# Kernel tuning notes

Hardware: AMD Instinct MI355X
Metric: run time of the kernel (lower is better)

The kernel has to match this reference:

```python
import jax, jax.numpy as jnp
import numpy as np

B, T, C = 4, 2048, 1024
H = 16
D = C // H  # head_dim = 64
SCALE = D ** -0.5


def setup_inputs() -> dict:
    key = jax.random.key(0)
    k1, k2, k3 = jax.random.split(key, 3)
    x = jax.random.normal(k1, (B, T, C), dtype=jnp.float32)
    w_qkv = jax.random.normal(k2, (C, 3 * C), dtype=jnp.float32) * (C ** -0.5)
    w_proj = jax.random.normal(k3, (C, C), dtype=jnp.float32) * (C ** -0.5)
    return {"x": x, "w_qkv": w_qkv, "w_proj": w_proj}


def reference(x, w_qkv, w_proj):
    Bx, Tx, Cx = x.shape
    qkv = x @ w_qkv                        # [B, T, 3C]
    q, k, v = jnp.split(qkv, 3, axis=-1)   # each [B, T, C]
    # [B, T, H, D] -> [B, H, T, D]
    q = q.reshape(Bx, Tx, H, D).transpose(0, 2, 1, 3)
    k = k.reshape(Bx, Tx, H, D).transpose(0, 2, 1, 3)
    v = v.reshape(Bx, Tx, H, D).transpose(0, 2, 1, 3)
    att = jnp.einsum('bhqd,bhkd->bhqk', q, k) * SCALE  # [B, H, T, T]
    causal = jnp.tril(jnp.ones((Tx, Tx), dtype=bool))
    att = jnp.where(causal[None, None], att, -jnp.inf)
    att = jax.nn.softmax(att, axis=-1)
    # dropout p=0.0 (eval-mode reference): identity
    y = jnp.einsum('bhqk,bhkd->bhqd', att, v)          # [B, H, T, D]
    y = y.transpose(0, 2, 1, 3).reshape(Bx, Tx, Cx)    # [B, T, C]
    return y @ w_proj
```

## Files before the change

### kernel.cpp

```cpp
#include <hip/hip_runtime.h>
#include <hip/hip_bf16.h>

#define Bdim 4
#define Tdim 2048
#define Cdim 1024
#define Hdim 16
#define Ddim 64
#define SCALE_Q 0.125f

using f32x4  = __attribute__((ext_vector_type(4))) float;
using short8 = __attribute__((ext_vector_type(8))) short;

union U8 { uint4 v; unsigned short s[8]; };

__device__ __forceinline__ float bf2f(unsigned short u) {
  union { unsigned int i; float f; } x; x.i = ((unsigned int)u) << 16; return x.f;
}
__device__ __forceinline__ unsigned short f2bf(float f) {
  union { float f; unsigned int i; } x; x.f = f;
  unsigned int lsb = (x.i >> 16) & 1u;
  unsigned int r = x.i + 0x7fffu + lsb;
  return (unsigned short)(r >> 16);
}

__device__ __forceinline__ void glds16(const unsigned short* g, unsigned short* l) {
  __builtin_amdgcn_global_load_lds(
      (const __attribute__((address_space(1))) void*)g,
      (__attribute__((address_space(3))) void*)l,
      16, 0, 0);
}

__device__ __forceinline__ int detect_fmt(const unsigned int* xw) {
  int cnt = 0;
  for (int i = 0; i < 64; i++) {
    unsigned int e = (xw[i] >> 7) & 0xFFu;
    if (e >= 100u && e <= 140u) cnt++;
  }
  return (cnt >= 40) ? 1 : 0;
}

__global__ void detect_kernel(const unsigned int* __restrict__ x, int* __restrict__ flag) {
  if (threadIdx.x == 0) *flag = detect_fmt(x);
}

__global__ __launch_bounds__(256) void prep_kernel(
    const void* __restrict__ x, const void* __restrict__ wq, const void* __restrict__ wp,
    unsigned short* __restrict__ X16, unsigned short* __restrict__ WqT,
    unsigned short* __restrict__ WpT, int* __restrict__ flag)
{
  __shared__ __align__(16) unsigned short Ts[64][72];
  __shared__ int sfmt;
  if (threadIdx.x == 0) {
    const int f = detect_fmt((const unsigned int*)x);
    sfmt = f;
    if (blockIdx.x == 0) *flag = f;
  }
  __syncthreads();
  const int fmt = sfmt;
  const unsigned bid = blockIdx.x;
  const int tid = threadIdx.x;

  if (bid < 4096u) {
    const size_t i = (size_t)bid * 256 + tid;
    if (fmt == 1) {
      *(uint4*)(X16 + i * 8) = *(const uint4*)((const unsigned short*)x + i * 8);
    } else {
      const float* s = (const float*)x + i * 8;
      float4 a = *(const float4*)(s);
      float4 b = *(const float4*)(s + 4);
      U8 o;
      o.s[0]=f2bf(a.x); o.s[1]=f2bf(a.y); o.s[2]=f2bf(a.z); o.s[3]=f2bf(a.w);
      o.s[4]=f2bf(b.x); o.s[5]=f2bf(b.y); o.s[6]=f2bf(b.z); o.s[7]=f2bf(b.w);
      *(uint4*)(X16 + i * 8) = o.v;
    }
    return;
  }

  const void* W; unsigned short* WT; int N, K, n0, k0;
  if (bid < 4864u) {
    const int t = bid - 4096;
    W = wq; WT = WqT; N = 3072; K = 1024;
    n0 = (t % 48) * 64; k0 = (t / 48) * 64;
  } else {
    const int t = bid - 4864;
    W = wp; WT = WpT; N = 1024; K = 1024;
    n0 = (t & 15) * 64; k0 = (t >> 4) * 64;
  }
  const int r = tid >> 2, c0 = (tid & 3) * 16;

  if (fmt == 0) {
    const float* Wf = (const float*)W + (size_t)(k0 + r) * N + n0 + c0;
    #pragma unroll
    for (int j4 = 0; j4 < 4; j4++) {
      float4 v = *(const float4*)(Wf + j4 * 4);
      Ts[r][c0 + j4*4 + 0] = f2bf(v.x);
      Ts[r][c0 + j4*4 + 1] = f2bf(v.y);
      Ts[r][c0 + j4*4 + 2] = f2bf(v.z);
      Ts[r][c0 + j4*4 + 3] = f2bf(v.w);
    }
  } else {
    const unsigned short* Wh = (const unsigned short*)W + (size_t)(k0 + r) * N + n0 + c0;
    uint4 v0 = *(const uint4*)(Wh);
    uint4 v1 = *(const uint4*)(Wh + 8);
    *(uint4*)&Ts[r][c0] = v0;
    *(uint4*)&Ts[r][c0 + 8] = v1;
  }
  __syncthreads();

  U8 o0, o1;
  #pragma unroll
  for (int j = 0; j < 8; j++) { o0.s[j] = Ts[c0 + j][r]; o1.s[j] = Ts[c0 + 8 + j][r]; }
  unsigned short* dst = WT + (size_t)(n0 + r) * K + k0 + c0;
  *(uint4*)(dst)     = o0.v;
  *(uint4*)(dst + 8) = o1.v;
}

__global__ __launch_bounds__(256) void vtrans_kernel(
    const unsigned short* __restrict__ Vb, unsigned short* __restrict__ VbT)
{
  __shared__ __align__(16) unsigned short Ts[64][72];
  const int tid = threadIdx.x;
  const int head = blockIdx.x >> 5;
  const int tt   = blockIdx.x & 31;
  const int r = tid >> 2, c0 = (tid & 3) * 16;

  const unsigned short* src = Vb + (size_t)head * Tdim * Ddim + (size_t)(tt * 64 + r) * Ddim + c0;
  uint4 a = *(const uint4*)(src);
  uint4 b = *(const uint4*)(src + 8);
  *(uint4*)&Ts[r][c0]     = a;
  *(uint4*)&Ts[r][c0 + 8] = b;
  __syncthreads();

  U8 o0, o1;
  #pragma unroll
  for (int j = 0; j < 8; j++) { o0.s[j] = Ts[c0 + j][r]; o1.s[j] = Ts[c0 + 8 + j][r]; }
  unsigned short* dst = VbT + (size_t)head * Tdim * Ddim + (size_t)r * Tdim + tt * 64 + c0;
  *(uint4*)(dst)     = o0.v;
  *(uint4*)(dst + 8) = o1.v;
}

__global__ __launch_bounds__(256) void gemm128b_kernel(
    const unsigned short* __restrict__ A16,
    const unsigned short* __restrict__ BT16,
    void* __restrict__ Cout,
    unsigned short* __restrict__ Qb,
    unsigned short* __restrict__ Kb,
    unsigned short* __restrict__ Vb,
    const int* __restrict__ flag,
    int M, int N, int K, int mode)
{
  __shared__ __align__(16) unsigned short As[2][128 * 32];
  __shared__ __align__(16) unsigned short Bs[2][128 * 32];

  const int fmt = *flag;
  const int tid  = threadIdx.x;
  const int wave = tid >> 6;
  const int lane = tid & 63;
  const int col  = lane & 15;
  const int quad = lane >> 4;
  const int m0 = blockIdx.x * 128;
  const int n0 = blockIdx.y * 128;
  const int wm = (wave >> 1) * 64;
  const int wn = (wave & 1) * 64;

  const int lr = lane >> 2;
  const int lc = (lane & 3) * 8;

  f32x4 acc[4][4];
  #pragma unroll
  for (int i = 0; i < 4; i++)
    #pragma unroll
    for (int j = 0; j < 4; j++) acc[i][j] = (f32x4){0.f, 0.f, 0.f, 0.f};

  const unsigned short* Ap0 = A16  + (size_t)(m0 + wave * 32 + lr) * K + lc;
  const unsigned short* Ap1 = A16  + (size_t)(m0 + wave * 32 + 16 + lr) * K + lc;
  const unsigned short* Bp0 = BT16 + (size_t)(n0 + wave * 32 + lr) * K + lc;
  const unsigned short* Bp1 = BT16 + (size_t)(n0 + wave * 32 + 16 + lr) * K + lc;
  unsigned short* a0 = &As[0][wave * 32 * 32];
  unsigned short* a0b = &As[0][(wave * 32 + 16) * 32];
  unsigned short* a1 = &As[1][wave * 32 * 32];
  unsigned short* a1b = &As[1][(wave * 32 + 16) * 32];
  unsigned short* b0 = &Bs[0][wave * 32 * 32];
  unsigned short* b0b = &Bs[0][(wave * 32 + 16) * 32];
  unsigned short* b1 = &Bs[1][wave * 32 * 32];
  unsigned short* b1b = &Bs[1][(wave * 32 + 16) * 32];

  for (int k0 = 0; k0 < K; k0 += 64) {
    glds16(Ap0,      a0);  glds16(Ap0 + 32, a1);
    glds16(Ap1,      a0b); glds16(Ap1 + 32, a1b);
    glds16(Bp0,      b0);  glds16(Bp0 + 32, b1);
    glds16(Bp1,      b0b); glds16(Bp1 + 32, b1b);
    Ap0 += 64; Ap1 += 64; Bp0 += 64; Bp1 += 64;
    __syncthreads();

    #pragma unroll
    for (int half = 0; half < 2; half++) {
      short8 afr[4], bfr[4];
      #pragma unroll
      for (int mi = 0; mi < 4; mi++)
        afr[mi] = *(const short8*)&As[half][(wm + mi * 16 + col) * 32 + quad * 8];
      #pragma unroll
      for (int ni = 0; ni < 4; ni++)
        bfr[ni] = *(const short8*)&Bs[half][(wn + ni * 16 + col) * 32 + quad * 8];
      #pragma unroll
      for (int mi = 0; mi < 4; mi++)
        #pragma unroll
        for (int ni = 0; ni < 4; ni++)
          acc[mi][ni] = __builtin_amdgcn_mfma_f32_16x16x32_bf16(afr[mi], bfr[ni], acc[mi][ni], 0, 0, 0);
    }
    __syncthreads();
  }

  if (mode == 1) {
    const int bb = m0 >> 11;
    const int tBase = (m0 & 2047) + wm;
    #pragma unroll
    for (int ni = 0; ni < 4; ni++) {
      const int n = n0 + wn + ni * 16 + col;
      const int which = n >> 10;
      const int rem = n & 1023;
      const int h = rem >> 6;
      const int d = rem & 63;
      unsigned short* dstBase = (which == 0) ? Qb : (which == 1 ? Kb : Vb);
      const float scale = (which == 0) ? SCALE_Q : 1.f;
      dstBase += (size_t)(bb * Hdim + h) * Tdim * Ddim + d;
      #pragma unroll
      for (int mi = 0; mi < 4; mi++)
        #pragma unroll
        for (int i = 0; i < 4; i++) {
          const int t = tBase + mi * 16 + quad * 4 + i;
          dstBase[(size_t)t * Ddim] = f2bf(acc[mi][ni][i] * scale);
        }
    }
  } else {
    #pragma unroll
    for (int mi = 0; mi < 4; mi++)
      #pragma unroll
      for (int ni = 0; ni < 4; ni++)
        #pragma unroll
        for (int i = 0; i < 4; i++) {
          const int m = m0 + wm + mi * 16 + quad * 4 + i;
          const int n = n0 + wn + ni * 16 + col;
          const float v = acc[mi][ni][i];
          if (fmt == 0) ((float*)Cout)[(size_t)m * N + n] = v;
          else ((unsigned short*)Cout)[(size_t)m * N + n] = f2bf(v);
        }
  }
}

#define XBM 128
#define XBN 128
#define XBK 32
#define XLDK 40

__global__ __launch_bounds__(256) void gemm128_kernel(
    const unsigned short* __restrict__ A16,
    const void* __restrict__ Bsrc,
    void* __restrict__ Cout,
    unsigned short* __restrict__ Qb,
    unsigned short* __restrict__ Kb,
    unsigned short* __restrict__ Vb,
    const int* __restrict__ flag,
    int M, int N, int K, int mode, int bFmt)
{
  __shared__ __align__(16) unsigned short As[XBM * XLDK];
  __shared__ __align__(16) unsigned short Bs[XBN * XLDK];

  const int fmt = *flag;
  const int tid  = threadIdx.x;
  const int wave = tid >> 6;
  const int lane = tid & 63;
  const int col  = lane & 15;
  const int quad = lane >> 4;
  const int m0 = blockIdx.x * XBM;
  const int n0 = blockIdx.y * XBN;
  const int wm = (wave >> 1) * 64;
  const int wn = (wave & 1) * 64;

  const int ar = tid >> 1;
  const int ah = (tid & 1) * 16;

  f32x4 acc[4][4];
  #pragma unroll
  for (int i = 0; i < 4; i++)
    #pragma unroll
    for (int j = 0; j < 4; j++) acc[i][j] = (f32x4){0.f, 0.f, 0.f, 0.f};

  for (int k0 = 0; k0 < K; k0 += XBK) {
    {
      const unsigned short* Ap = A16 + (size_t)(m0 + ar) * K + k0 + ah;
      uint4 a0 = *(const uint4*)(Ap);
      uint4 a1 = *(const uint4*)(Ap + 8);
      *(uint4*)&As[ar * XLDK + ah]     = a0;
      *(uint4*)&As[ar * XLDK + ah + 8] = a1;
    }
    if (bFmt == 1) {
      const unsigned short* Bp = (const unsigned short*)Bsrc + (size_t)(n0 + ar) * K + k0 + ah;
      uint4 b0 = *(const uint4*)(Bp);
      uint4 b1 = *(const uint4*)(Bp + 8);
      *(uint4*)&Bs[ar * XLDK + ah]     = b0;
      *(uint4*)&Bs[ar * XLDK + ah + 8] = b1;
    } else {
      const int bn = tid & 127;
      const int bg = (tid >> 7) * 16;
      U8 p0, p1;
      if (fmt == 0) {
        const float* Bf = (const float*)Bsrc;
        #pragma unroll
        for (int j = 0; j < 8; j++) {
          p0.s[j] = f2bf(Bf[(size_t)(k0 + bg + j) * N + n0 + bn]);
          p1.s[j] = f2bf(Bf[(size_t)(k0 + bg + 8 + j) * N + n0 + bn]);
        }
      } else {
        const unsigned short* Bh = (const unsigned short*)Bsrc;
        #pragma unroll
        for (int j = 0; j < 8; j++) {
          p0.s[j] = Bh[(size_t)(k0 + bg + j) * N + n0 + bn];
          p1.s[j] = Bh[(size_t)(k0 + bg + 8 + j) * N + n0 + bn];
        }
      }
      *(uint4*)&Bs[bn * XLDK + bg]     = p0.v;
      *(uint4*)&Bs[bn * XLDK + bg + 8] = p1.v;
    }
    __syncthreads();

    short8 afr[4], bfr[4];
    #pragma unroll
    for (int mi = 0; mi < 4; mi++)
      afr[mi] = *(const short8*)&As[(wm + mi * 16 + col) * XLDK + quad * 8];
    #pragma unroll
    for (int ni = 0; ni < 4; ni++)
      bfr[ni] = *(const short8*)&Bs[(wn + ni * 16 + col) * XLDK + quad * 8];
    #pragma unroll
    for (int mi = 0; mi < 4; mi++)
      #pragma unroll
      for (int ni = 0; ni < 4; ni++)
        acc[mi][ni] = __builtin_amdgcn_mfma_f32_16x16x32_bf16(afr[mi], bfr[ni], acc[mi][ni], 0, 0, 0);
    __syncthreads();
  }

  #pragma unroll
  for (int mi = 0; mi < 4; mi++) {
    #pragma unroll
    for (int ni = 0; ni < 4; ni++) {
      #pragma unroll
      for (int i = 0; i < 4; i++) {
        const int m = m0 + wm + mi * 16 + quad * 4 + i;
        const int n = n0 + wn + ni * 16 + col;
        const float v = acc[mi][ni][i];
        if (mode == 0) {
          if (fmt == 0) ((float*)Cout)[(size_t)m * N + n] = v;
          else ((unsigned short*)Cout)[(size_t)m * N + n] = f2bf(v);
        } else {
          const int which = n >> 10;
          const int rem = n & 1023;
          const int h = rem >> 6;
          const int d = rem & 63;
          const int b = m >> 11;
          const int t = m & 2047;
          const size_t idx = ((size_t)(b * Hdim + h) * Tdim + t) * Ddim + d;
          if      (which == 0) Qb[idx] = f2bf(v * SCALE_Q);
          else if (which == 1) Kb[idx] = f2bf(v);
          else                 Vb[idx] = f2bf(v);
        }
      }
    }
  }
}

#define BM 64
#define BN 64
#define BK 32
#define LDK 40

__global__ __launch_bounds__(256) void gemm64_kernel(
    const void* __restrict__ A,
    const void* __restrict__ Bw,
    void* __restrict__ Cout,
    unsigned short* __restrict__ Qb,
    unsigned short* __restrict__ Kb,
    unsigned short* __restrict__ Vb,
    const int* __restrict__ flag,
    int M, int N, int K, int mode, int aFmt, int outFmt, int aOff, int mOff)
{
  __shared__ __align__(16) unsigned short As[BM * LDK];
  __shared__ __align__(16) unsigned short Bs[BN * LDK];

  const int fmt = *flag;
  const int af  = (aFmt  == 2) ? fmt : aFmt;
  const int of  = (outFmt == 2) ? fmt : outFmt;

  const int tid  = threadIdx.x;
  const int wave = tid >> 6;
  const int lane = tid & 63;
  const int m0 = blockIdx.x * BM;
  const int n0 = blockIdx.y * BN;

  const int ar = tid >> 2;
  const int ak = (tid & 3) * 8;
  const int bk = tid >> 3;
  const int bn = (tid & 7) * 8;

  const int lr = lane & 15;
  const int lq = lane >> 4;

  f32x4 acc[4] = {{0,0,0,0},{0,0,0,0},{0,0,0,0},{0,0,0,0}};

  for (int k0 = 0; k0 < K; k0 += BK) {
    U8 a8;
    if (af == 1) {
      a8.v = *(const uint4*)((const unsigned short*)A + (size_t)(aOff + m0 + ar) * K + (k0 + ak));
    } else {
      const float* Af = (const float*)A + (size_t)(aOff + m0 + ar) * K + (k0 + ak);
      float4 x0 = *(const float4*)(Af);
      float4 x1 = *(const float4*)(Af + 4);
      a8.s[0] = f2bf(x0.x); a8.s[1] = f2bf(x0.y); a8.s[2] = f2bf(x0.z); a8.s[3] = f2bf(x0.w);
      a8.s[4] = f2bf(x1.x); a8.s[5] = f2bf(x1.y); a8.s[6] = f2bf(x1.z); a8.s[7] = f2bf(x1.w);
    }
    *(uint4*)(&As[ar * LDK + ak]) = a8.v;

    U8 b8;
    if (fmt == 1) {
      b8.v = *(const uint4*)((const unsigned short*)Bw + (size_t)(k0 + bk) * N + (n0 + bn));
    } else {
      const float* Bf = (const float*)Bw + (size_t)(k0 + bk) * N + (n0 + bn);
      float4 x0 = *(const float4*)(Bf);
      float4 x1 = *(const float4*)(Bf + 4);
      b8.s[0] = f2bf(x0.x); b8.s[1] = f2bf(x0.y); b8.s[2] = f2bf(x0.z); b8.s[3] = f2bf(x0.w);
      b8.s[4] = f2bf(x1.x); b8.s[5] = f2bf(x1.y); b8.s[6] = f2bf(x1.z); b8.s[7] = f2bf(x1.w);
    }
    #pragma unroll
    for (int i = 0; i < 8; i++) Bs[(bn + i) * LDK + bk] = b8.s[i];
    __syncthreads();

    short8 afrag = *(const short8*)(&As[(wave * 16 + lr) * LDK + lq * 8]);
    #pragma unroll
    for (int c = 0; c < 4; c++) {
      short8 bfrag = *(const short8*)(&Bs[(c * 16 + lr) * LDK + lq * 8]);
      acc[c] = __builtin_amdgcn_mfma_f32_16x16x32_bf16(afrag, bfrag, acc[c], 0, 0, 0);
    }
    __syncthreads();
  }

  #pragma unroll
  for (int c = 0; c < 4; c++) {
    #pragma unroll
    for (int i = 0; i < 4; i++) {
      const int m = m0 + wave * 16 + lq * 4 + i;
      const int n = n0 + c * 16 + lr;
      const float v = acc[c][i];
      if (mode == 0) {
        if (of == 0) ((float*)Cout)[(size_t)(mOff + m) * N + n] = v;
        else ((unsigned short*)Cout)[(size_t)(mOff + m) * N + n] = f2bf(v);
      } else {
        const int which = n >> 10;
        const int rem = n & 1023;
        const int h = rem >> 6;
        const int d = rem & 63;
        const int b = m >> 11;
        const int t = m & 2047;
        const size_t idx = ((size_t)(b * Hdim + h) * Tdim + t) * Ddim + d;
        if      (which == 0) Qb[idx] = f2bf(v * SCALE_Q);
        else if (which == 1) Kb[idx] = f2bf(v);
        else                 Vb[idx] = f2bf(v);
      }
    }
  }
}

__global__ __launch_bounds__(256) void attn128_kernel(
    const unsigned short* __restrict__ Qb,
    const unsigned short* __restrict__ Kb,
    const unsigned short* __restrict__ Vb,
    const unsigned short* __restrict__ VbT,
    unsigned short* __restrict__ Y)
{
  __shared__ __align__(16) unsigned short Ks[64 * 72];
  __shared__ __align__(16) unsigned short Vt[64 * 72];
  __shared__ __align__(16) unsigned short Pw[4][32 * 72];

  const int tid  = threadIdx.x;
  const int wave = tid >> 6;
  const int lane = tid & 63;
  const int col  = lane & 15;
  const int quad = lane >> 4;

  const int pair = blockIdx.x & 7;
  const int bh   = blockIdx.x >> 3;
  const size_t headOff = (size_t)bh * Tdim * Ddim;

  const int sr = tid >> 2;
  const int sc = (tid & 3) * 16;

  const int b = bh >> 4;
  const int h = bh & 15;

  #pragma unroll
  for (int half = 0; half < 2; half++) {
    const int qt = half ? (15 - pair) : pair;
    const int qb = qt * 128;
    const int nkt = (qb >> 6) + 2;
    const int rMin = qb + wave * 32;
    const int rMax = rMin + 31;

    short8 qf[2][2];
    #pragma unroll
    for (int mi = 0; mi < 2; mi++) {
      const unsigned short* Qr = Qb + headOff + (size_t)(rMin + mi * 16 + col) * Ddim;
      qf[mi][0] = *(const short8*)(Qr + quad * 8);
      qf[mi][1] = *(const short8*)(Qr + 32 + quad * 8);
    }

    f32x4 o_acc[2][4];
    float l_i[2][4];
    #pragma unroll
    for (int mi = 0; mi < 2; mi++)
      #pragma unroll
      for (int n = 0; n < 4; n++) {
        o_acc[mi][n] = (f32x4){0.f, 0.f, 0.f, 0.f};
        l_i[mi][n] = 0.f;
      }

    uint4 kr0, kr1, vr0, vr1;
    {
      const unsigned short* Kr = Kb + headOff + (size_t)sr * Ddim + sc;
      kr0 = *(const uint4*)(Kr);
      kr1 = *(const uint4*)(Kr + 8);
      if (VbT) {
        const unsigned short* Vr = VbT + headOff + (size_t)sr * Tdim + sc;
        vr0 = *(const uint4*)(Vr);
        vr1 = *(const uint4*)(Vr + 8);
      } else {
        const unsigned short* Vr = Vb + headOff + (size_t)sr * Ddim + sc;
        vr0 = *(const uint4*)(Vr);
        vr1 = *(const uint4*)(Vr + 8);
      }
    }

    for (int kt = 0; kt < nkt; kt++) {
      __syncthreads();
      *(uint4*)&Ks[sr * 72 + sc]     = kr0;
      *(uint4*)&Ks[sr * 72 + sc + 8] = kr1;
      if (VbT) {
        *(uint4*)&Vt[sr * 72 + sc]     = vr0;
        *(uint4*)&Vt[sr * 72 + sc + 8] = vr1;
      } else {
        U8 v0, v1; v0.v = vr0; v1.v = vr1;
        #pragma unroll
        for (int j = 0; j < 8; j++) {
          Vt[(sc + j) * 72 + sr]     = v0.s[j];
          Vt[(sc + 8 + j) * 72 + sr] = v1.s[j];
        }
      }
      __syncthreads();

      if (kt + 1 < nkt) {
        const int kb = (kt + 1) * 64;
        const unsigned short* Kr = Kb + headOff + (size_t)(kb + sr) * Ddim + sc;
        kr0 = *(const uint4*)(Kr);
        kr1 = *(const uint4*)(Kr + 8);
        if (VbT) {
          const unsigned short* Vr = VbT + headOff + (size_t)sr * Tdim + kb + sc;
          vr0 = *(const uint4*)(Vr);
          vr1 = *(const uint4*)(Vr + 8);
        } else {
          const unsigned short* Vr = Vb + headOff + (size_t)(kb + sr) * Ddim + sc;
          vr0 = *(const uint4*)(Vr);
          vr1 = *(const uint4*)(Vr + 8);
        }
      }

      const int ktb = kt * 64;
      if (ktb <= rMax) {
        f32x4 s_acc[2][4];
        #pragma unroll
        for (int c = 0; c < 4; c++) {
          const unsigned short* Kl = &Ks[(c * 16 + col) * 72];
          short8 kf0 = *(const short8*)(Kl + quad * 8);
          short8 kf1 = *(const short8*)(Kl + 32 + quad * 8);
          #pragma unroll
          for (int mi = 0; mi < 2; mi++) {
            f32x4 z = {0.f, 0.f, 0.f, 0.f};
            z = __builtin_amdgcn_mfma_f32_16x16x32_bf16(qf[mi][0], kf0, z, 0, 0, 0);
            s_acc[mi][c] = __builtin_amdgcn_mfma_f32_16x16x32_bf16(qf[mi][1], kf1, z, 0, 0, 0);
          }
        }

        if (ktb + 63 > rMin) {
          #pragma unroll
          for (int mi = 0; mi < 2; mi++)
            #pragma unroll
            for (int c = 0; c < 4; c++)
              #pragma unroll
              for (int i = 0; i < 4; i++)
                if (ktb + c * 16 + col > rMin + mi * 16 + quad * 4 + i)
                  s_acc[mi][c][i] = -1e30f;
        }

        #pragma unroll
        for (int mi = 0; mi < 2; mi++)
          #pragma unroll
          for (int c = 0; c < 4; c++)
            #pragma unroll
            for (int i = 0; i < 4; i++) {
              const float p = __expf(fminf(s_acc[mi][c][i], 60.f));
              l_i[mi][i] += p;
              Pw[wave][(mi * 16 + quad * 4 + i) * 72 + c * 16 + col] = f2bf(p);
            }

        short8 pf[2][2];
        #pragma unroll
        for (int mi = 0; mi < 2; mi++) {
          pf[mi][0] = *(const short8*)(&Pw[wave][(mi * 16 + col) * 72 + quad * 8]);
          pf[mi][1] = *(const short8*)(&Pw[wave][(mi * 16 + col) * 72 + 32 + quad * 8]);
        }
        #pragma unroll
        for (int n = 0; n < 4; n++) {
          const unsigned short* Vl = &Vt[(n * 16 + col) * 72];
          short8 vf0 = *(const short8*)(Vl + quad * 8);
          short8 vf1 = *(const short8*)(Vl + 32 + quad * 8);
          #pragma unroll
          for (int mi = 0; mi < 2; mi++) {
            o_acc[mi][n] = __builtin_amdgcn_mfma_f32_16x16x32_bf16(pf[mi][0], vf0, o_acc[mi][n], 0, 0, 0);
            o_acc[mi][n] = __builtin_amdgcn_mfma_f32_16x16x32_bf16(pf[mi][1], vf1, o_acc[mi][n], 0, 0, 0);
          }
        }
      }
    }
    __syncthreads();

    #pragma unroll
    for (int mi = 0; mi < 2; mi++)
      #pragma unroll
      for (int i = 0; i < 4; i++) {
        float s = l_i[mi][i];
        s += __shfl_xor(s, 1);
        s += __shfl_xor(s, 2);
        s += __shfl_xor(s, 4);
        s += __shfl_xor(s, 8);
        const float inv = 1.f / s;
        const int qrow = rMin + mi * 16 + quad * 4 + i;
        unsigned short* dst = Y + (size_t)(b * Tdim + qrow) * Cdim + h * Ddim;
        #pragma unroll
        for (int n = 0; n < 4; n++)
          dst[n * 16 + col] = f2bf(o_acc[mi][n][i] * inv);
      }
  }
}

extern "C" void kernel_launch(void* const* d_in, const int* in_sizes, int n_in,
                              void* d_out, int out_size, void* d_ws, size_t ws_size,
                              hipStream_t stream) {
  const void* x      = d_in[0];
  const void* w_qkv  = d_in[1];
  const void* w_proj = d_in[2];

  int* flag = (int*)d_ws;
  unsigned short* wsb = (unsigned short*)((char*)d_ws + 1024);

  const size_t HS = (size_t)Bdim * Hdim * Tdim * Ddim;
  const size_t FULL  = 1024 + 2 * (4 * HS + (size_t)3072 * 1024 + (size_t)1024 * 1024);
  const size_t FULL2 = FULL + 2 * HS;
  const size_t MONO  = 1024 + 2 * (4 * HS);

  dim3 blk(256);

  if (ws_size >= FULL) {
    unsigned short* Qb  = wsb;
    unsigned short* Kb  = Qb + HS;
    unsigned short* Vb  = Kb + HS;
    unsigned short* XY  = Vb + HS;
    unsigned short* WqT = XY + HS;
    unsigned short* WpT = WqT + (size_t)3072 * 1024;
    unsigned short* VbT = WpT + (size_t)1024 * 1024;
    const int M = Bdim * Tdim;

    prep_kernel<<<dim3(5120), blk, 0, stream>>>(x, w_qkv, w_proj, XY, WqT, WpT, flag);

    gemm128b_kernel<<<dim3(M / 128, 3072 / 128), blk, 0, stream>>>(
        XY, WqT, nullptr, Qb, Kb, Vb, flag, M, 3072, Cdim, 1);

    if (ws_size >= FULL2) {
      vtrans_kernel<<<dim3(Bdim * Hdim * (Tdim / 64)), blk, 0, stream>>>(Vb, VbT);
      attn128_kernel<<<dim3(Bdim * Hdim * 8), blk, 0, stream>>>(Qb, Kb, Vb, VbT, XY);
    } else {
      attn128_kernel<<<dim3(Bdim * Hdim * 8), blk, 0, stream>>>(Qb, Kb, Vb, nullptr, XY);
    }

    gemm128b_kernel<<<dim3(M / 128, Cdim / 128), blk, 0, stream>>>(
        XY, WpT, d_out, nullptr, nullptr, nullptr, flag, M, Cdim, Cdim, 0);
  } else if (ws_size >= MONO) {
    unsigned short* Qb  = wsb;
    unsigned short* Kb  = Qb + HS;
    unsigned short* Vb  = Kb + HS;
    unsigned short* XY  = Vb + HS;
    const int M = Bdim * Tdim;

    detect_kernel<<<1, 64, 0, stream>>>((const unsigned int*)x, flag);

    {
      const size_t n8 = (size_t)M * Cdim / 8;
      (void)n8;
    }

    const size_t HSb = (size_t)Hdim * Tdim * Ddim;
    unsigned short* Qb2 = wsb;
    unsigned short* Kb2 = Qb2 + HSb;
    unsigned short* Vb2 = Kb2 + HSb;
    unsigned short* Y2  = Vb2 + HSb;
    for (int b = 0; b < Bdim; b++) {
      gemm64_kernel<<<dim3(Tdim / BM, 3072 / BN), blk, 0, stream>>>(
          x, w_qkv, nullptr, Qb2, Kb2, Vb2, flag,
          Tdim, 3072, Cdim, 1, 2, 2, b * Tdim, 0);
      attn128_kernel<<<dim3(Hdim * 8), blk, 0, stream>>>(Qb2, Kb2, Vb2, nullptr, Y2);
      gemm64_kernel<<<dim3(Tdim / BM, Cdim / BN), blk, 0, stream>>>(
          Y2, w_proj, d_out, nullptr, nullptr, nullptr, flag,
          Tdim, Cdim, Cdim, 0, 1, 2, 0, b * Tdim);
    }
  } else {
    detect_kernel<<<1, 64, 0, stream>>>((const unsigned int*)x, flag);
    const size_t HSb = (size_t)Hdim * Tdim * Ddim;
    unsigned short* Qb = wsb;
    unsigned short* Kb = Qb + HSb;
    unsigned short* Vb = Kb + HSb;
    unsigned short* Y2 = Vb + HSb;

    for (int b = 0; b < Bdim; b++) {
      gemm64_kernel<<<dim3(Tdim / BM, 3072 / BN), blk, 0, stream>>>(
          x, w_qkv, nullptr, Qb, Kb, Vb, flag,
          Tdim, 3072, Cdim, 1, 2, 2, b * Tdim, 0);

      attn128_kernel<<<dim3(Hdim * 8), blk, 0, stream>>>(Qb, Kb, Vb, nullptr, Y2);

      gemm64_kernel<<<dim3(Tdim / BM, Cdim / BN), blk, 0, stream>>>(
          Y2, w_proj, d_out, nullptr, nullptr, nullptr, flag,
          Tdim, Cdim, Cdim, 0, 1, 2, 0, b * Tdim);
    }
  }
}
```

Before: 273.4 us.

## Split attention blocks per query tile, transpose S, use exp2 and MFMA row sums

```diff
diff --git a/kernel.cpp b/kernel.cpp
--- a/kernel.cpp
+++ b/kernel.cpp
@@ -6,7 +6,7 @@
 #define Cdim 1024
 #define Hdim 16
 #define Ddim 64
-#define SCALE_Q 0.125f
+#define SCALE_Q 0.18033688011112042f
 
 using f32x4  = __attribute__((ext_vector_type(4))) float;
 using short8 = __attribute__((ext_vector_type(8))) short;
@@ -21,6 +21,14 @@
   unsigned int lsb = (x.i >> 16) & 1u;
   unsigned int r = x.i + 0x7fffu + lsb;
   return (unsigned short)(r >> 16);
+}
+
+__device__ __forceinline__ float fexp2(float x) {
+#if __has_builtin(__builtin_amdgcn_exp2f)
+  return __builtin_amdgcn_exp2f(x);
+#else
+  return exp2f(x);
+#endif
 }
 
 __device__ __forceinline__ void glds16(const unsigned short* g, unsigned short* l) {
@@ -485,8 +493,9 @@
   const int col  = lane & 15;
   const int quad = lane >> 4;
 
-  const int pair = blockIdx.x & 7;
-  const int bh   = blockIdx.x >> 3;
+  const int t    = blockIdx.x & 15;
+  const int bh   = blockIdx.x >> 4;
+  const int qt   = (t & 1) ? (15 - (t >> 1)) : (t >> 1);
   const size_t headOff = (size_t)bh * Tdim * Ddim;
 
   const int sr = tid >> 2;
@@ -495,157 +504,153 @@
   const int b = bh >> 4;
   const int h = bh & 15;
 
-  #pragma unroll
-  for (int half = 0; half < 2; half++) {
-    const int qt = half ? (15 - pair) : pair;
-    const int qb = qt * 128;
-    const int nkt = (qb >> 6) + 2;
-    const int rMin = qb + wave * 32;
-    const int rMax = rMin + 31;
-
-    short8 qf[2][2];
-    #pragma unroll
-    for (int mi = 0; mi < 2; mi++) {
-      const unsigned short* Qr = Qb + headOff + (size_t)(rMin + mi * 16 + col) * Ddim;
-      qf[mi][0] = *(const short8*)(Qr + quad * 8);
-      qf[mi][1] = *(const short8*)(Qr + 32 + quad * 8);
-    }
-
-    f32x4 o_acc[2][4];
-    float l_i[2][4];
-    #pragma unroll
-    for (int mi = 0; mi < 2; mi++)
-      #pragma unroll
-      for (int n = 0; n < 4; n++) {
-        o_acc[mi][n] = (f32x4){0.f, 0.f, 0.f, 0.f};
-        l_i[mi][n] = 0.f;
-      }
-
-    uint4 kr0, kr1, vr0, vr1;
-    {
-      const unsigned short* Kr = Kb + headOff + (size_t)sr * Ddim + sc;
+  const int qb = qt * 128;
+  const int nkt = (qb >> 6) + 2;
+  const int rMin = qb + wave * 32;
+  const int rMax = rMin + 31;
+
+  short8 qf[2][2];
+  #pragma unroll
+  for (int mi = 0; mi < 2; mi++) {
+    const unsigned short* Qr = Qb + headOff + (size_t)(rMin + mi * 16 + col) * Ddim;
+    qf[mi][0] = *(const short8*)(Qr + quad * 8);
+    qf[mi][1] = *(const short8*)(Qr + 32 + quad * 8);
+  }
+
+  const short8 onesf = {16256, 16256, 16256, 16256, 16256, 16256, 16256, 16256};
+
+  f32x4 o_acc[2][4];
+  f32x4 l_acc[2];
+  #pragma unroll
+  for (int mi = 0; mi < 2; mi++) {
+    l_acc[mi] = (f32x4){0.f, 0.f, 0.f, 0.f};
+    #pragma unroll
+    for (int n = 0; n < 4; n++) o_acc[mi][n] = (f32x4){0.f, 0.f, 0.f, 0.f};
+  }
+
+  uint4 kr0, kr1, vr0, vr1;
+  {
+    const unsigned short* Kr = Kb + headOff + (size_t)sr * Ddim + sc;
+    kr0 = *(const uint4*)(Kr);
+    kr1 = *(const uint4*)(Kr + 8);
+    if (VbT) {
+      const unsigned short* Vr = VbT + headOff + (size_t)sr * Tdim + sc;
+      vr0 = *(const uint4*)(Vr);
+      vr1 = *(const uint4*)(Vr + 8);
+    } else {
+      const unsigned short* Vr = Vb + headOff + (size_t)sr * Ddim + sc;
+      vr0 = *(const uint4*)(Vr);
+      vr1 = *(const uint4*)(Vr + 8);
+    }
+  }
+
+  for (int kt = 0; kt < nkt; kt++) {
+    __syncthreads();
+    *(uint4*)&Ks[sr * 72 + sc]     = kr0;
+    *(uint4*)&Ks[sr * 72 + sc + 8] = kr1;
+    if (VbT) {
+      *(uint4*)&Vt[sr * 72 + sc]     = vr0;
+      *(uint4*)&Vt[sr * 72 + sc + 8] = vr1;
+    } else {
+      U8 v0, v1; v0.v = vr0; v1.v = vr1;
+      #pragma unroll
+      for (int j = 0; j < 8; j++) {
+        Vt[(sc + j) * 72 + sr]     = v0.s[j];
+        Vt[(sc + 8 + j) * 72 + sr] = v1.s[j];
+      }
+    }
+    __syncthreads();
+
+    if (kt + 1 < nkt) {
+      const int kb = (kt + 1) * 64;
+      const unsigned short* Kr = Kb + headOff + (size_t)(kb + sr) * Ddim + sc;
       kr0 = *(const uint4*)(Kr);
       kr1 = *(const uint4*)(Kr + 8);
       if (VbT) {
-        const unsigned short* Vr = VbT + headOff + (size_t)sr * Tdim + sc;
+        const unsigned short* Vr = VbT + headOff + (size_t)sr * Tdim + kb + sc;
         vr0 = *(const uint4*)(Vr);
         vr1 = *(const uint4*)(Vr + 8);
       } else {
-        const unsigned short* Vr = Vb + headOff + (size_t)sr * Ddim + sc;
+        const unsigned short* Vr = Vb + headOff + (size_t)(kb + sr) * Ddim + sc;
         vr0 = *(const uint4*)(Vr);
         vr1 = *(const uint4*)(Vr + 8);
       }
     }
 
-    for (int kt = 0; kt < nkt; kt++) {
-      __syncthreads();
-      *(uint4*)&Ks[sr * 72 + sc]     = kr0;
-      *(uint4*)&Ks[sr * 72 + sc + 8] = kr1;
-      if (VbT) {
-        *(uint4*)&Vt[sr * 72 + sc]     = vr0;
-        *(uint4*)&Vt[sr * 72 + sc + 8] = vr1;
-      } else {
-        U8 v0, v1; v0.v = vr0; v1.v = vr1;
-        #pragma unroll
-        for (int j = 0; j < 8; j++) {
-          Vt[(sc + j) * 72 + sr]     = v0.s[j];
-          Vt[(sc + 8 + j) * 72 + sr] = v1.s[j];
+    const int ktb = kt * 64;
+    if (ktb <= rMax) {
+      f32x4 s_acc[4][2];
+      #pragma unroll
+      for (int c = 0; c < 4; c++) {
+        const unsigned short* Kl = &Ks[(c * 16 + col) * 72];
+        short8 kf0 = *(const short8*)(Kl + quad * 8);
+        short8 kf1 = *(const short8*)(Kl + 32 + quad * 8);
+        #pragma unroll
+        for (int mi = 0; mi < 2; mi++) {
+          f32x4 z = {0.f, 0.f, 0.f, 0.f};
+          z = __builtin_amdgcn_mfma_f32_16x16x32_bf16(kf0, qf[mi][0], z, 0, 0, 0);
+          s_acc[c][mi] = __builtin_amdgcn_mfma_f32_16x16x32_bf16(kf1, qf[mi][1], z, 0, 0, 0);
         }
       }
-      __syncthreads();
-
-      if (kt + 1 < nkt) {
-        const int kb = (kt + 1) * 64;
-        const unsigned short* Kr = Kb + headOff + (size_t)(kb + sr) * Ddim + sc;
-        kr0 = *(const uint4*)(Kr);
-        kr1 = *(const uint4*)(Kr + 8);
-        if (VbT) {
-          const unsigned short* Vr = VbT + headOff + (size_t)sr * Tdim + kb + sc;
-          vr0 = *(const uint4*)(Vr);
-          vr1 = *(const uint4*)(Vr + 8);
-        } else {
-          const unsigned short* Vr = Vb + headOff + (size_t)(kb + sr) * Ddim + sc;
-          vr0 = *(const uint4*)(Vr);
-          vr1 = *(const uint4*)(Vr + 8);
-        }
-      }
-
-      const int ktb = kt * 64;
-      if (ktb <= rMax) {
-        f32x4 s_acc[2][4];
-        #pragma unroll
-        for (int c = 0; c < 4; c++) {
-          const unsigned short* Kl = &Ks[(c * 16 + col) * 72];
-          short8 kf0 = *(const short8*)(Kl + quad * 8);
-          short8 kf1 = *(const short8*)(Kl + 32 + quad * 8);
-          #pragma unroll
-          for (int mi = 0; mi < 2; mi++) {
-            f32x4 z = {0.f, 0.f, 0.f, 0.f};
-            z = __builtin_amdgcn_mfma_f32_16x16x32_bf16(qf[mi][0], kf0, z, 0, 0, 0);
-            s_acc[mi][c] = __builtin_amdgcn_mfma_f32_16x16x32_bf16(qf[mi][1], kf1, z, 0, 0, 0);
-          }
-        }
-
-        if (ktb + 63 > rMin) {
+
+      if (ktb + 63 > rMin) {
+        #pragma unroll
+        for (int c = 0; c < 4; c++)
           #pragma unroll
           for (int mi = 0; mi < 2; mi++)
             #pragma unroll
-            for (int c = 0; c < 4; c++)
-              #pragma unroll
-              for (int i = 0; i < 4; i++)
-                if (ktb + c * 16 + col > rMin + mi * 16 + quad * 4 + i)
-                  s_acc[mi][c][i] = -1e30f;
+            for (int i = 0; i < 4; i++)
+              if (ktb + c * 16 + quad * 4 + i > rMin + mi * 16 + col)
+                s_acc[c][mi][i] = -1e30f;
+      }
+
+      #pragma unroll
+      for (int mi = 0; mi < 2; mi++)
+        #pragma unroll
+        for (int c = 0; c < 4; c++) {
+          const float p0 = fexp2(fminf(s_acc[c][mi][0], 80.f));
+          const float p1 = fexp2(fminf(s_acc[c][mi][1], 80.f));
+          const float p2 = fexp2(fminf(s_acc[c][mi][2], 80.f));
+          const float p3 = fexp2(fminf(s_acc[c][mi][3], 80.f));
+          const unsigned int u0 = (unsigned int)f2bf(p0) | ((unsigned int)f2bf(p1) << 16);
+          const unsigned int u1 = (unsigned int)f2bf(p2) | ((unsigned int)f2bf(p3) << 16);
+          uint2* dst = (uint2*)&Pw[wave][(mi * 16 + col) * 72 + c * 16 + quad * 4];
+          *dst = make_uint2(u0, u1);
         }
 
-        #pragma unroll
-        for (int mi = 0; mi < 2; mi++)
-          #pragma unroll
-          for (int c = 0; c < 4; c++)
-            #pragma unroll
-            for (int i = 0; i < 4; i++) {
-              const float p = __expf(fminf(s_acc[mi][c][i], 60.f));
-              l_i[mi][i] += p;
-              Pw[wave][(mi * 16 + quad * 4 + i) * 72 + c * 16 + col] = f2bf(p);
-            }
-
-        short8 pf[2][2];
+      short8 pf[2][2];
+      #pragma unroll
+      for (int mi = 0; mi < 2; mi++) {
+        pf[mi][0] = *(const short8*)(&Pw[wave][(mi * 16 + col) * 72 + quad * 8]);
+        pf[mi][1] = *(const short8*)(&Pw[wave][(mi * 16 + col) * 72 + 32 + quad * 8]);
+        l_acc[mi] = __builtin_amdgcn_mfma_f32_16x16x32_bf16(pf[mi][0], onesf, l_acc[mi], 0, 0, 0);
+        l_acc[mi] = __builtin_amdgcn_mfma_f32_16x16x32_bf16(pf[mi][1], onesf, l_acc[mi], 0, 0, 0);
+      }
+      #pragma unroll
+      for (int n = 0; n < 4; n++) {
+        const unsigned short* Vl = &Vt[(n * 16 + col) * 72];
+        short8 vf0 = *(const short8*)(Vl + quad * 8);
+        short8 vf1 = *(const short8*)(Vl + 32 + quad * 8);
         #pragma unroll
         for (int mi = 0; mi < 2; mi++) {
-          pf[mi][0] = *(const short8*)(&Pw[wave][(mi * 16 + col) * 72 + quad * 8]);
-          pf[mi][1] = *(const short8*)(&Pw[wave][(mi * 16 + col) * 72 + 32 + quad * 8]);
+          o_acc[mi][n] = __builtin_amdgcn_mfma_f32_16x16x32_bf16(pf[mi][0], vf0, o_acc[mi][n], 0, 0, 0);
+          o_acc[mi][n] = __builtin_amdgcn_mfma_f32_16x16x32_bf16(pf[mi][1], vf1, o_acc[mi][n], 0, 0, 0);
         }
-        #pragma unroll
-        for (int n = 0; n < 4; n++) {
-          const unsigned short* Vl = &Vt[(n * 16 + col) * 72];
-          short8 vf0 = *(const short8*)(Vl + quad * 8);
-          short8 vf1 = *(const short8*)(Vl + 32 + quad * 8);
-          #pragma unroll
-          for (int mi = 0; mi < 2; mi++) {
-            o_acc[mi][n] = __builtin_amdgcn_mfma_f32_16x16x32_bf16(pf[mi][0], vf0, o_acc[mi][n], 0, 0, 0);
-            o_acc[mi][n] = __builtin_amdgcn_mfma_f32_16x16x32_bf16(pf[mi][1], vf1, o_acc[mi][n], 0, 0, 0);
-          }
-        }
-      }
-    }
-    __syncthreads();
-
-    #pragma unroll
-    for (int mi = 0; mi < 2; mi++)
-      #pragma unroll
-      for (int i = 0; i < 4; i++) {
-        float s = l_i[mi][i];
-        s += __shfl_xor(s, 1);
-        s += __shfl_xor(s, 2);
-        s += __shfl_xor(s, 4);
-        s += __shfl_xor(s, 8);
-        const float inv = 1.f / s;
-        const int qrow = rMin + mi * 16 + quad * 4 + i;
-        unsigned short* dst = Y + (size_t)(b * Tdim + qrow) * Cdim + h * Ddim;
-        #pragma unroll
-        for (int n = 0; n < 4; n++)
-          dst[n * 16 + col] = f2bf(o_acc[mi][n][i] * inv);
-      }
-  }
+      }
+    }
+  }
+
+  #pragma unroll
+  for (int mi = 0; mi < 2; mi++)
+    #pragma unroll
+    for (int i = 0; i < 4; i++) {
+      const float inv = 1.f / l_acc[mi][i];
+      const int qrow = rMin + mi * 16 + quad * 4 + i;
+      unsigned short* dst = Y + (size_t)(b * Tdim + qrow) * Cdim + h * Ddim;
+      #pragma unroll
+      for (int n = 0; n < 4; n++)
+        dst[n * 16 + col] = f2bf(o_acc[mi][n][i] * inv);
+    }
 }
 
 extern "C" void kernel_launch(void* const* d_in, const int* in_sizes, int n_in,
@@ -682,27 +687,15 @@
 
     if (ws_size >= FULL2) {
       vtrans_kernel<<<dim3(Bdim * Hdim * (Tdim / 64)), blk, 0, stream>>>(Vb, VbT);
-      attn128_kernel<<<dim3(Bdim * Hdim * 8), blk, 0, stream>>>(Qb, Kb, Vb, VbT, XY);
+      attn128_kernel<<<dim3(Bdim * Hdim * 16), blk, 0, stream>>>(Qb, Kb, Vb, VbT, XY);
     } else {
-      attn128_kernel<<<dim3(Bdim * Hdim * 8), blk, 0, stream>>>(Qb, Kb, Vb, nullptr, XY);
+      attn128_kernel<<<dim3(Bdim * Hdim * 16), blk, 0, stream>>>(Qb, Kb, Vb, nullptr, XY);
     }
 
     gemm128b_kernel<<<dim3(M / 128, Cdim / 128), blk, 0, stream>>>(
         XY, WpT, d_out, nullptr, nullptr, nullptr, flag, M, Cdim, Cdim, 0);
   } else if (ws_size >= MONO) {
-    unsigned short* Qb  = wsb;
-    unsigned short* Kb  = Qb + HS;
-    unsigned short* Vb  = Kb + HS;
-    unsigned short* XY  = Vb + HS;
-    const int M = Bdim * Tdim;
-
     detect_kernel<<<1, 64, 0, stream>>>((const unsigned int*)x, flag);
-
-    {
-      const size_t n8 = (size_t)M * Cdim / 8;
-      (void)n8;
-    }
-
     const size_t HSb = (size_t)Hdim * Tdim * Ddim;
     unsigned short* Qb2 = wsb;
     unsigned short* Kb2 = Qb2 + HSb;
@@ -712,7 +705,7 @@
       gemm64_kernel<<<dim3(Tdim / BM, 3072 / BN), blk, 0, stream>>>(
           x, w_qkv, nullptr, Qb2, Kb2, Vb2, flag,
           Tdim, 3072, Cdim, 1, 2, 2, b * Tdim, 0);
-      attn128_kernel<<<dim3(Hdim * 8), blk, 0, stream>>>(Qb2, Kb2, Vb2, nullptr, Y2);
+      attn128_kernel<<<dim3(Hdim * 16), blk, 0, stream>>>(Qb2, Kb2, Vb2, nullptr, Y2);
       gemm64_kernel<<<dim3(Tdim / BM, Cdim / BN), blk, 0, stream>>>(
           Y2, w_proj, d_out, nullptr, nullptr, nullptr, flag,
           Tdim, Cdim, Cdim, 0, 1, 2, 0, b * Tdim);
@@ -730,7 +723,7 @@
           x, w_qkv, nullptr, Qb, Kb, Vb, flag,
           Tdim, 3072, Cdim, 1, 2, 2, b * Tdim, 0);
 
-      attn128_kernel<<<dim3(Hdim * 8), blk, 0, stream>>>(Qb, Kb, Vb, nullptr, Y2);
+      attn128_kernel<<<dim3(Hdim * 16), blk, 0, stream>>>(Qb, Kb, Vb, nullptr, Y2);
 
       gemm64_kernel<<<dim3(Tdim / BM, Cdim / BN), blk, 0, stream>>>(
           Y2, w_proj, d_out, nullptr, nullptr, nullptr, flag,
```

New measurement: 313.8 us. 14.8% more time.
